# Optimization experiments

Measured on AMD Instinct MI355X. Metric: run time of the kernel, lower is better.

The kernel has to match this reference:

```python
import jax, jax.numpy as jnp
import numpy as np

B, N, C = 8, 2048, 256
NGRP = 4          # n oscillator dims per group
RANK = 16         # A_rank
EPS = 1e-6        # solver eps
GN_EPS = 1e-5     # torch GroupNorm default eps


def setup_inputs() -> dict:
    key = jax.random.key(0)
    k0, k1, k2, k3 = jax.random.split(key, 4)
    x = jax.random.normal(k0, (B, N, C), jnp.float32)
    y = jax.random.normal(k1, (B, C, N), jnp.float32)
    sc = jax.random.uniform(k2, (B, N, N), jnp.float32)
    U = 0.01 * jax.random.normal(k3, (N, RANK), jnp.float32)
    omega_param = (1.0 / np.sqrt(2)).astype(np.float32) * jnp.ones((C // 2, 1), jnp.float32)
    gn_w = jnp.ones((C,), jnp.float32)
    gn_b = jnp.zeros((C,), jnp.float32)
    gamma = jnp.float32(1.0)
    return {"x": x, "y": y, "sc": sc, "U": U, "omega_param": omega_param,
            "gn_w": gn_w, "gn_b": gn_b, "gamma": gamma, "Q": 8}


def _map_to_sphere(x):
    # normalize each group of NGRP channels to unit norm
    xv = x.reshape(B, N, C // NGRP, NGRP)
    n2 = jnp.clip(jnp.sum(xv * xv, axis=-1, keepdims=True), EPS, None)
    return (xv * jax.lax.rsqrt(n2)).reshape(B, N, C)


def _project_osc(v, x):
    # remove component of v along x within each oscillator group (tangent projection)
    xv = x.reshape(B, N, C // NGRP, NGRP)
    vv = v.reshape(B, N, C // NGRP, NGRP)
    sim = jnp.sum(xv * vv, axis=-1, keepdims=True)
    return (vv - sim * xv).reshape(B, N, C)


def _group_norm(y, w, b):
    # y: [B, C, N]; num_groups = C // NGRP, NGRP channels per group
    G = C // NGRP
    yv = y.reshape(B, G, NGRP * N)
    mu = jnp.mean(yv, axis=-1, keepdims=True)
    var = jnp.mean((yv - mu) ** 2, axis=-1, keepdims=True)
    yn = ((yv - mu) * jax.lax.rsqrt(var + GN_EPS)).reshape(B, C, N)
    return yn * w[None, :, None] + b[None, :, None]


def _omega_term(x, omega_param):
    # pairwise rotation: (x0, x1) -> (omg*x1, -omg*x0), omg = |omega_param| per pair
    xp = x.reshape(B, N, C // 2, 2)
    omg = jnp.abs(omega_param).reshape(1, 1, C // 2)  # norm over trailing dim of size 1
    out = jnp.stack([omg * xp[..., 1], -omg * xp[..., 0]], axis=-1)
    return out.reshape(B, N, C)


def _kuramoto(x, y, sc, U, omega_param, gn_w, gn_b, gamma, Q):
    rho = 1.0
    # y: [B, C, N] -> GroupNorm -> [B, N, C] -> sphere
    y = _group_norm(y, gn_w, gn_b)
    y = _map_to_sphere(jnp.transpose(y, (0, 2, 1)))
    # x: [B, N, C] (N != C so no transpose in original)
    x = _map_to_sphere(x)
    # coupling matrix K = sym(W) * sigmoid(U U^T)  (normalize_K=False, w_scale=1)
    Wsym = 0.5 * (sc + jnp.transpose(sc, (0, 2, 1)))
    A = jax.nn.sigmoid(U @ U.T)          # [N, N]
    K = Wsym * A[None, :, :]             # [B, N, N]

    def step(xc, _):
        coupling = jnp.einsum('bnm,bmc->bnc', K, xc)
        force = coupling + y
        om = _omega_term(xc, omega_param)
        dxdt = om + rho * _project_osc(force, xc)
        xn = _map_to_sphere(xc + gamma * dxdt)
        return xn, xn

    _, xs = jax.lax.scan(step, x, None, length=Q)
    return xs  # [Q, B, N, C]


def reference(x, y, sc, U, omega_param, gn_w, gn_b, gamma, Q):
    return _kuramoto(x, y, sc, U, omega_param, gn_w, gn_b, gamma, Q)
```

## Files before the change

kernel.cpp:

```cpp
#include <hip/hip_runtime.h>
#include <hip/hip_bf16.h>

#define BB 8
#define NN 2048
#define CC 256
#define GG 64
#define QQ 8

typedef unsigned short u16;
typedef __attribute__((ext_vector_type(8))) short bf16x8;
typedef __attribute__((ext_vector_type(4))) float f32x4;

static __device__ __forceinline__ float b2f(u16 u) {
  union { unsigned int i; float f; } cv; cv.i = ((unsigned int)u) << 16; return cv.f;
}
static __device__ __forceinline__ u16 f2b(float f) {
  union { __hip_bfloat16 h; u16 u; } cv; cv.h = __float2bfloat16(f); return cv.u;
}
static __device__ __forceinline__ float ldin(const void* p, size_t i, bool f32) {
  return f32 ? ((const float*)p)[i] : b2f(((const u16*)p)[i]);
}
static __device__ __forceinline__ float4 ldin4(const void* p, size_t i, bool f32) {
  if (f32) return *(const float4*)((const float*)p + i);
  ushort4 u = *(const ushort4*)((const u16*)p + i);
  return make_float4(b2f(u.x), b2f(u.y), b2f(u.z), b2f(u.w));
}
static __device__ __forceinline__ void gload16(const void* g, void* l) {
  __builtin_amdgcn_global_load_lds(
      (const __attribute__((address_space(1))) void*)g,
      (__attribute__((address_space(3))) void*)l, 16, 0, 0);
}

__global__ __launch_bounds__(256) void detect_kernel(const u16* __restrict__ sc,
                                                     int* __restrict__ flag)
{
  __shared__ int sh;
  if (threadIdx.x == 0) sh = 0;
  __syncthreads();
  int cnt = 0;
  for (int i = threadIdx.x; i < 2048; i += 256) {
    u16 w = sc[2 * i];
    int e = (w >> 7) & 0xFF;
    if (e >= 100 && e <= 130) cnt++;
  }
  atomicAdd(&sh, cnt);
  __syncthreads();
  if (threadIdx.x == 0) *flag = (sh < 1024) ? 1 : 0;
}

__global__ __launch_bounds__(256) void build_k_kernel(
    const void* __restrict__ sc, const void* __restrict__ U,
    u16* __restrict__ Khi, u16* __restrict__ Klo,
    const int* __restrict__ flagp, int grp)
{
  const int i0 = blockIdx.y * 32;
  const int j0 = blockIdx.x * 32;
  if (j0 < i0) return;
  const bool f32 = (*flagp != 0);
  const int tx = threadIdx.x;
  const int ty = threadIdx.y;
  const int t  = ty * 32 + tx;
  const int rr = t >> 3;
  const int cq = t & 7;

  __shared__ float Ui[32][17];
  __shared__ float Uj[32][17];
  __shared__ float As[32][33];
  __shared__ float t1[32][33];
  __shared__ float t2[32][33];

  for (int s = t; s < 512; s += 256) {
    int r2 = s >> 4, kk = s & 15;
    Ui[r2][kk] = ldin(U, (size_t)(i0 + r2) * 16 + kk, f32);
    Uj[r2][kk] = ldin(U, (size_t)(j0 + r2) * 16 + kk, f32);
  }
  __syncthreads();
  for (int ii = ty; ii < 32; ii += 8) {
    float dot = 0.f;
    #pragma unroll
    for (int k = 0; k < 16; k++) dot += Ui[ii][k] * Uj[tx][k];
    As[ii][tx] = 1.0f / (1.0f + expf(-dot));
  }

  for (int bl = 0; bl < 4; bl++) {
    const int b = grp * 4 + bl;
    const size_t scb = (size_t)b * NN * NN;
    __syncthreads();
    float4 va = ldin4(sc, scb + (size_t)(i0 + rr) * NN + j0 + 4 * cq, f32);
    float4 vb = ldin4(sc, scb + (size_t)(j0 + rr) * NN + i0 + 4 * cq, f32);
    t1[rr][4*cq+0] = va.x; t1[rr][4*cq+1] = va.y;
    t1[rr][4*cq+2] = va.z; t1[rr][4*cq+3] = va.w;
    t2[rr][4*cq+0] = vb.x; t2[rr][4*cq+1] = vb.y;
    t2[rr][4*cq+2] = vb.z; t2[rr][4*cq+3] = vb.w;
    __syncthreads();
    const size_t kfb = (size_t)bl * NN * NN;
    ushort4 h4, l4;
    #pragma unroll
    for (int k = 0; k < 4; k++) {
      int col = 4 * cq + k;
      float kv = 0.5f * (t1[rr][col] + t2[col][rr]) * As[rr][col];
      u16 h = f2b(kv);
      ((u16*)&h4)[k] = h;
      ((u16*)&l4)[k] = f2b(kv - b2f(h));
    }
    size_t o = kfb + (size_t)(i0 + rr) * NN + j0 + 4 * cq;
    *(ushort4*)(Khi + o) = h4;
    *(ushort4*)(Klo + o) = l4;
    if (i0 != j0) {
      #pragma unroll
      for (int k = 0; k < 4; k++) {
        int col = 4 * cq + k;
        float kv = 0.5f * (t2[rr][col] + t1[col][rr]) * As[col][rr];
        u16 h = f2b(kv);
        ((u16*)&h4)[k] = h;
        ((u16*)&l4)[k] = f2b(kv - b2f(h));
      }
      size_t o2 = kfb + (size_t)(j0 + rr) * NN + i0 + 4 * cq;
      *(ushort4*)(Khi + o2) = h4;
      *(ushort4*)(Klo + o2) = l4;
    }
  }
}

__global__ __launch_bounds__(256) void gn_stats_kernel(
    const void* __restrict__ y, float* __restrict__ murs,
    const int* __restrict__ flagp)
{
  const bool f32 = (*flagp != 0);
  const int bg = blockIdx.x;
  float s = 0.f, ss = 0.f;
  if (f32) {
    const float* base = (const float*)y + (size_t)bg * 4 * NN;
    for (int i = threadIdx.x; i < 2048; i += 256) {
      float4 v = *(const float4*)(base + (size_t)i * 4);
      s  += v.x + v.y + v.z + v.w;
      ss += v.x*v.x + v.y*v.y + v.z*v.z + v.w*v.w;
    }
  } else {
    const u16* base = (const u16*)y + (size_t)bg * 4 * NN;
    for (int i = threadIdx.x; i < 2048; i += 256) {
      ushort4 v = *(const ushort4*)(base + (size_t)i * 4);
      float f0 = b2f(v.x), f1 = b2f(v.y), f2 = b2f(v.z), f3 = b2f(v.w);
      s  += f0 + f1 + f2 + f3;
      ss += f0*f0 + f1*f1 + f2*f2 + f3*f3;
    }
  }
  #pragma unroll
  for (int off = 32; off > 0; off >>= 1) {
    s  += __shfl_down(s, off, 64);
    ss += __shfl_down(ss, off, 64);
  }
  __shared__ float sh[8];
  const int w = threadIdx.x >> 6, ln = threadIdx.x & 63;
  if (ln == 0) { sh[w * 2] = s; sh[w * 2 + 1] = ss; }
  __syncthreads();
  if (threadIdx.x == 0) {
    float S  = sh[0] + sh[2] + sh[4] + sh[6];
    float SS = sh[1] + sh[3] + sh[5] + sh[7];
    float mu  = S / 8192.0f;
    float var = SS / 8192.0f - mu * mu;
    murs[bg * 2]     = mu;
    murs[bg * 2 + 1] = 1.0f / sqrtf(fmaxf(var, 0.f) + 1e-5f);
  }
}

__global__ __launch_bounds__(256) void y_tf_kernel(
    const void* __restrict__ y, const float* __restrict__ murs,
    const void* __restrict__ gw, const void* __restrict__ gb,
    float* __restrict__ yt, const int* __restrict__ flagp)
{
  const bool f32 = (*flagp != 0);
  const int b = blockIdx.y;
  const int n = blockIdx.x * 64 + threadIdx.x;
  for (int g = threadIdx.y; g < GG; g += 4) {
    float mu = murs[(b * GG + g) * 2];
    float rs = murs[(b * GG + g) * 2 + 1];
    float v[4];
    #pragma unroll
    for (int k = 0; k < 4; k++) {
      int c = 4 * g + k;
      float val = (ldin(y, ((size_t)b * CC + c) * NN + n, f32) - mu) * rs;
      v[k] = val * ldin(gw, c, f32) + ldin(gb, c, f32);
    }
    float n2 = v[0]*v[0] + v[1]*v[1] + v[2]*v[2] + v[3]*v[3];
    float scl = 1.0f / sqrtf(fmaxf(n2, 1e-6f));
    float4 o; o.x = v[0]*scl; o.y = v[1]*scl; o.z = v[2]*scl; o.w = v[3]*scl;
    *(float4*)(yt + ((size_t)b * NN + n) * CC + 4 * g) = o;
  }
}

__global__ __launch_bounds__(256) void x_init_kernel(
    const void* __restrict__ x, u16* __restrict__ xTh, u16* __restrict__ xTl,
    const int* __restrict__ flagp)
{
  const bool f32 = (*flagp != 0);
  const int b = blockIdx.y;
  const int n = blockIdx.x * 64 + threadIdx.x;
  for (int g = threadIdx.y; g < GG; g += 4) {
    size_t idx = ((size_t)b * NN + n) * CC + 4 * g;
    float v[4];
    if (f32) {
      float4 u4 = *(const float4*)((const float*)x + idx);
      v[0] = u4.x; v[1] = u4.y; v[2] = u4.z; v[3] = u4.w;
    } else {
      ushort4 u = *(const ushort4*)((const u16*)x + idx);
      v[0] = b2f(u.x); v[1] = b2f(u.y); v[2] = b2f(u.z); v[3] = b2f(u.w);
    }
    float n2 = v[0]*v[0] + v[1]*v[1] + v[2]*v[2] + v[3]*v[3];
    float scl = 1.0f / sqrtf(fmaxf(n2, 1e-6f));
    size_t xb = ((size_t)b * CC + 4 * g) * NN + n;
    #pragma unroll
    for (int k = 0; k < 4; k++) {
      float xv = v[k] * scl;
      u16 h = f2b(xv);
      xTh[xb + (size_t)k * NN] = h;
      xTl[xb + (size_t)k * NN] = f2b(xv - b2f(h));
    }
  }
}

__global__ __launch_bounds__(256, 2) void gemm_fused_kernel(
    const u16* __restrict__ Khi, const u16* __restrict__ Klo,
    const u16* __restrict__ xhc, const u16* __restrict__ xlc,
    u16* __restrict__ xhn, u16* __restrict__ xln,
    const float* __restrict__ yt, const void* __restrict__ omega,
    const void* __restrict__ gamma, void* __restrict__ outbase, size_t qoff,
    const int* __restrict__ flagp, int grp)
{
  const int flat = blockIdx.x + 4 * blockIdx.y + 128 * blockIdx.z;
  const int swz  = (flat & 7) * 64 + (flat >> 3);
  const int bx = swz & 3;
  const int by = (swz >> 2) & 31;
  const int bl = swz >> 7;
  const int b  = grp * 4 + bl;
  const int m0 = by * 64;
  const int c0 = bx * 64;

  __shared__ char lds[2][32768];

  const int t    = threadIdx.x;
  const int lane = t & 63;
  const int wid  = t >> 6;
  const int wr   = wid >> 1;
  const int wc   = wid & 1;

  const u16* Ah = Khi + (size_t)bl * NN * NN;
  const u16* Al = Klo + (size_t)bl * NN * NN;
  const u16* Bh = xhc + (size_t)b * CC * NN;
  const u16* Bl = xlc + (size_t)b * CC * NN;

  const int tr   = t >> 3;
  const int phys = (t & 7) ^ (tr & 7);
  const size_t aoff = (size_t)(m0 + tr) * NN + phys * 8;
  const size_t boff = (size_t)(c0 + tr) * NN + phys * 8;
  const int dst = wid * 1024;

  f32x4 acc[2][2];
  const f32x4 zero4 = {0.f, 0.f, 0.f, 0.f};
  #pragma unroll
  for (int i = 0; i < 2; i++)
    #pragma unroll
    for (int j = 0; j < 2; j++) acc[i][j] = zero4;

  auto stage = [&](int bufi, int k0) {
    char* base = &lds[bufi][0];
    #pragma unroll
    for (int i = 0; i < 2; i++) {
      gload16(Ah + aoff + (size_t)i * (32 * NN) + k0, base +         i * 4096 + dst);
      gload16(Al + aoff + (size_t)i * (32 * NN) + k0, base +  8192 + i * 4096 + dst);
      gload16(Bh + boff + (size_t)i * (32 * NN) + k0, base + 16384 + i * 4096 + dst);
      gload16(Bl + boff + (size_t)i * (32 * NN) + k0, base + 24576 + i * 4096 + dst);
    }
  };

  const int l15 = lane & 15;
  const int lk  = lane >> 4;

  auto compute = [&](int bufi) {
    const char* base = &lds[bufi][0];
    #pragma unroll
    for (int ks = 0; ks < 2; ks++) {
      const int cl = ks * 4 + lk;
      bf16x8 fah[2], fal[2], fbh[2], fbl[2];
      #pragma unroll
      for (int fr = 0; fr < 2; fr++) {
        int r   = wr * 32 + fr * 16 + l15;
        int off = r * 128 + ((cl ^ (r & 7)) << 4);
        fah[fr] = *(const bf16x8*)(base + off);
        fal[fr] = *(const bf16x8*)(base + 8192 + off);
      }
      #pragma unroll
      for (int fc = 0; fc < 2; fc++) {
        int r   = wc * 32 + fc * 16 + l15;
        int off = r * 128 + ((cl ^ (r & 7)) << 4);
        fbh[fc] = *(const bf16x8*)(base + 16384 + off);
        fbl[fc] = *(const bf16x8*)(base + 24576 + off);
      }
      #pragma unroll
      for (int fr = 0; fr < 2; fr++)
        #pragma unroll
        for (int fc = 0; fc < 2; fc++) {
          acc[fr][fc] = __builtin_amdgcn_mfma_f32_16x16x32_bf16(
              fah[fr], fbh[fc], acc[fr][fc], 0, 0, 0);
          acc[fr][fc] = __builtin_amdgcn_mfma_f32_16x16x32_bf16(
              fah[fr], fbl[fc], acc[fr][fc], 0, 0, 0);
          acc[fr][fc] = __builtin_amdgcn_mfma_f32_16x16x32_bf16(
              fal[fr], fbh[fc], acc[fr][fc], 0, 0, 0);
        }
    }
  };

  stage(0, 0);
  __syncthreads();
  int buf = 0;
  for (int kt = 0; kt < NN / 64; kt++) {
    if (kt + 1 < NN / 64) stage(buf ^ 1, (kt + 1) * 64);
    compute(buf);
    __syncthreads();
    buf ^= 1;
  }

  const bool f32 = (*flagp != 0);
  const float gm = ldin(gamma, 0, f32);
  #pragma unroll
  for (int fr = 0; fr < 2; fr++) {
    const int rbase = m0 + wr * 32 + fr * 16 + lk * 4;
    #pragma unroll
    for (int fc = 0; fc < 2; fc++) {
      const int c = c0 + wc * 32 + fc * 16 + l15;
      const size_t xoff = ((size_t)b * CC + c) * NN + rbase;
      ushort4 xh4 = *(const ushort4*)(xhc + xoff);
      ushort4 xl4 = *(const ushort4*)(xlc + xoff);
      float xcv[4] = { b2f(xh4.x) + b2f(xl4.x), b2f(xh4.y) + b2f(xl4.y),
                       b2f(xh4.z) + b2f(xl4.z), b2f(xh4.w) + b2f(xl4.w) };
      float om   = fabsf(ldin(omega, c >> 1, f32));
      float omsg = (c & 1) ? -om : om;
      float xn[4];
      #pragma unroll
      for (int r = 0; r < 4; r++) {
        const int n = rbase + r;
        float f = acc[fr][fc][r] + yt[((size_t)b * NN + n) * CC + c];
        float s = xcv[r] * f;
        s += __shfl_xor(s, 1);
        s += __shfl_xor(s, 2);
        float xp = __shfl_xor(xcv[r], 1);
        float d  = omsg * xp + (f - s * xcv[r]);
        float v  = xcv[r] + gm * d;
        float n2 = v * v;
        n2 += __shfl_xor(n2, 1);
        n2 += __shfl_xor(n2, 2);
        float scl = 1.0f / sqrtf(fmaxf(n2, 1e-6f));
        xn[r] = v * scl;
        const size_t oidx = qoff + ((size_t)b * NN + n) * CC + c;
        if (f32) ((float*)outbase)[oidx] = xn[r];
        else     ((u16*)outbase)[oidx]   = f2b(xn[r]);
      }
      ushort4 nh, nl;
      #pragma unroll
      for (int r = 0; r < 4; r++) {
        u16 h = f2b(xn[r]);
        ((u16*)&nh)[r] = h;
        ((u16*)&nl)[r] = f2b(xn[r] - b2f(h));
      }
      *(ushort4*)(xhn + xoff) = nh;
      *(ushort4*)(xln + xoff) = nl;
    }
  }
}

extern "C" void kernel_launch(void* const* d_in, const int* in_sizes, int n_in,
                              void* d_out, int out_size, void* d_ws, size_t ws_size,
                              hipStream_t stream) {
  const void* x     = d_in[0];
  const void* y     = d_in[1];
  const void* sc    = d_in[2];
  const void* U     = d_in[3];
  const void* omega = d_in[4];
  const void* gw    = d_in[5];
  const void* gb    = d_in[6];
  const void* gamma = d_in[7];
  char* ws = (char*)d_ws;

  const size_t BNC = (size_t)BB * NN * CC;
  u16*   Khi  = (u16*)(ws);
  u16*   Klo  = (u16*)(ws + 33554432);
  float* yt   = (float*)(ws + 67108864);
  u16*   xAh  = (u16*)(ws + 83886080);
  u16*   xAl  = (u16*)(ws + 92274688);
  u16*   xBh  = (u16*)(ws + 100663296);
  u16*   xBl  = (u16*)(ws + 109051904);
  float* murs = (float*)(ws + 117440512);
  int*   flag = (int*)  (ws + 117444608);

  u16* xh[2] = { xAh, xBh };
  u16* xl[2] = { xAl, xBl };

  detect_kernel<<<dim3(1), dim3(256), 0, stream>>>((const u16*)sc, flag);
  gn_stats_kernel<<<dim3(512), dim3(256), 0, stream>>>(y, murs, flag);
  y_tf_kernel<<<dim3(32, 8), dim3(64, 4), 0, stream>>>(y, murs, gw, gb, yt, flag);
  x_init_kernel<<<dim3(32, 8), dim3(64, 4), 0, stream>>>(x, xAh, xAl, flag);

  for (int grp = 0; grp < 2; grp++) {
    build_k_kernel<<<dim3(64, 64), dim3(32, 8), 0, stream>>>(
        sc, U, Khi, Klo, flag, grp);
    for (int q = 0; q < QQ; q++) {
      const int cur = q & 1, nxt = cur ^ 1;
      gemm_fused_kernel<<<dim3(4, 32, 4), dim3(256), 0, stream>>>(
          Khi, Klo, xh[cur], xl[cur], xh[nxt], xl[nxt],
          yt, omega, gamma, d_out, (size_t)q * BNC, flag, grp);
    }
  }
}
```

Measured before the change: 916.3 us.

## Load B operand fragments directly from global into registers, halve LDS

```diff
diff --git a/kernel.cpp b/kernel.cpp
--- a/kernel.cpp
+++ b/kernel.cpp
@@ -236,7 +236,7 @@
   const int m0 = by * 64;
   const int c0 = bx * 64;
 
-  __shared__ char lds[2][32768];
+  __shared__ char lds[2][16384];
 
   const int t    = threadIdx.x;
   const int lane = t & 63;
@@ -252,8 +252,15 @@
   const int tr   = t >> 3;
   const int phys = (t & 7) ^ (tr & 7);
   const size_t aoff = (size_t)(m0 + tr) * NN + phys * 8;
-  const size_t boff = (size_t)(c0 + tr) * NN + phys * 8;
   const int dst = wid * 1024;
+
+  const int l15 = lane & 15;
+  const int lk  = lane >> 4;
+
+  const u16* bh0 = Bh + (size_t)(c0 + wc * 32 +      l15) * NN + lk * 8;
+  const u16* bh1 = Bh + (size_t)(c0 + wc * 32 + 16 + l15) * NN + lk * 8;
+  const u16* bl0 = Bl + (size_t)(c0 + wc * 32 +      l15) * NN + lk * 8;
+  const u16* bl1 = Bl + (size_t)(c0 + wc * 32 + 16 + l15) * NN + lk * 8;
 
   f32x4 acc[2][2];
   const f32x4 zero4 = {0.f, 0.f, 0.f, 0.f};
@@ -262,26 +269,32 @@
     #pragma unroll
     for (int j = 0; j < 2; j++) acc[i][j] = zero4;
 
-  auto stage = [&](int bufi, int k0) {
+  auto stageA = [&](int bufi, int kt) {
     char* base = &lds[bufi][0];
-    #pragma unroll
-    for (int i = 0; i < 2; i++) {
-      gload16(Ah + aoff + (size_t)i * (32 * NN) + k0, base +         i * 4096 + dst);
-      gload16(Al + aoff + (size_t)i * (32 * NN) + k0, base +  8192 + i * 4096 + dst);
-      gload16(Bh + boff + (size_t)i * (32 * NN) + k0, base + 16384 + i * 4096 + dst);
-      gload16(Bl + boff + (size_t)i * (32 * NN) + k0, base + 24576 + i * 4096 + dst);
-    }
+    const int k0 = kt * 64;
+    gload16(Ah + aoff + k0,           base +         dst);
+    gload16(Ah + aoff + 32 * NN + k0, base +  4096 + dst);
+    gload16(Al + aoff + k0,           base +  8192 + dst);
+    gload16(Al + aoff + 32 * NN + k0, base + 12288 + dst);
   };
 
-  const int l15 = lane & 15;
-  const int lk  = lane >> 4;
-
-  auto compute = [&](int bufi) {
+  auto loadB = [&](bf16x8 (&fh)[2][2], bf16x8 (&fl)[2][2], int kt) {
+    const int k0 = kt * 64;
+    #pragma unroll
+    for (int ks = 0; ks < 2; ks++) {
+      fh[ks][0] = *(const bf16x8*)(bh0 + k0 + ks * 32);
+      fh[ks][1] = *(const bf16x8*)(bh1 + k0 + ks * 32);
+      fl[ks][0] = *(const bf16x8*)(bl0 + k0 + ks * 32);
+      fl[ks][1] = *(const bf16x8*)(bl1 + k0 + ks * 32);
+    }
+  };
+
+  auto computeA = [&](int bufi, bf16x8 (&fh)[2][2], bf16x8 (&fl)[2][2]) {
     const char* base = &lds[bufi][0];
     #pragma unroll
     for (int ks = 0; ks < 2; ks++) {
       const int cl = ks * 4 + lk;
-      bf16x8 fah[2], fal[2], fbh[2], fbl[2];
+      bf16x8 fah[2], fal[2];
       #pragma unroll
       for (int fr = 0; fr < 2; fr++) {
         int r   = wr * 32 + fr * 16 + l15;
@@ -290,34 +303,34 @@
         fal[fr] = *(const bf16x8*)(base + 8192 + off);
       }
       #pragma unroll
-      for (int fc = 0; fc < 2; fc++) {
-        int r   = wc * 32 + fc * 16 + l15;
-        int off = r * 128 + ((cl ^ (r & 7)) << 4);
-        fbh[fc] = *(const bf16x8*)(base + 16384 + off);
-        fbl[fc] = *(const bf16x8*)(base + 24576 + off);
-      }
-      #pragma unroll
       for (int fr = 0; fr < 2; fr++)
         #pragma unroll
         for (int fc = 0; fc < 2; fc++) {
           acc[fr][fc] = __builtin_amdgcn_mfma_f32_16x16x32_bf16(
-              fah[fr], fbh[fc], acc[fr][fc], 0, 0, 0);
+              fah[fr], fh[ks][fc], acc[fr][fc], 0, 0, 0);
           acc[fr][fc] = __builtin_amdgcn_mfma_f32_16x16x32_bf16(
-              fah[fr], fbl[fc], acc[fr][fc], 0, 0, 0);
+              fah[fr], fl[ks][fc], acc[fr][fc], 0, 0, 0);
           acc[fr][fc] = __builtin_amdgcn_mfma_f32_16x16x32_bf16(
-              fal[fr], fbh[fc], acc[fr][fc], 0, 0, 0);
+              fal[fr], fh[ks][fc], acc[fr][fc], 0, 0, 0);
         }
     }
   };
 
-  stage(0, 0);
+  bf16x8 b0h[2][2], b0l[2][2], b1h[2][2], b1l[2][2];
+  stageA(0, 0);
+  loadB(b0h, b0l, 0);
   __syncthreads();
-  int buf = 0;
-  for (int kt = 0; kt < NN / 64; kt++) {
-    if (kt + 1 < NN / 64) stage(buf ^ 1, (kt + 1) * 64);
-    compute(buf);
+  for (int kt = 0; kt < NN / 64; kt += 2) {
+    stageA(1, kt + 1);
+    loadB(b1h, b1l, kt + 1);
+    computeA(0, b0h, b0l);
     __syncthreads();
-    buf ^= 1;
+    if (kt + 2 < NN / 64) {
+      stageA(0, kt + 2);
+      loadB(b0h, b0l, kt + 2);
+    }
+    computeA(1, b1h, b1l);
+    __syncthreads();
   }
 
   const bool f32 = (*flagp != 0);
```

New measurement: 1.687 ms. +84.1%, slower.

## Process all batches per launch with single-buffered higher-occupancy GEMM when workspace allows

Applied to the files above, without the earlier changes.

```diff
diff --git a/kernel.cpp b/kernel.cpp
--- a/kernel.cpp
+++ b/kernel.cpp
@@ -51,7 +51,7 @@
 __global__ __launch_bounds__(256) void build_k_kernel(
     const void* __restrict__ sc, const void* __restrict__ U,
     u16* __restrict__ Khi, u16* __restrict__ Klo,
-    const int* __restrict__ flagp, int grp)
+    const int* __restrict__ flagp, int b0, int nbat)
 {
   const int i0 = blockIdx.y * 32;
   const int j0 = blockIdx.x * 32;
@@ -82,8 +82,8 @@
     As[ii][tx] = 1.0f / (1.0f + expf(-dot));
   }
 
-  for (int bl = 0; bl < 4; bl++) {
-    const int b = grp * 4 + bl;
+  for (int bl = 0; bl < nbat; bl++) {
+    const int b = b0 + bl;
     const size_t scb = (size_t)b * NN * NN;
     __syncthreads();
     float4 va = ldin4(sc, scb + (size_t)(i0 + rr) * NN + j0 + 4 * cq, f32);
@@ -219,108 +219,14 @@
   }
 }
 
-__global__ __launch_bounds__(256, 2) void gemm_fused_kernel(
-    const u16* __restrict__ Khi, const u16* __restrict__ Klo,
+static __device__ __forceinline__ void fused_step_epilogue(
+    f32x4 (&acc)[2][2], int b, int m0, int c0, int wr, int wc, int l15, int lk,
     const u16* __restrict__ xhc, const u16* __restrict__ xlc,
     u16* __restrict__ xhn, u16* __restrict__ xln,
     const float* __restrict__ yt, const void* __restrict__ omega,
     const void* __restrict__ gamma, void* __restrict__ outbase, size_t qoff,
-    const int* __restrict__ flagp, int grp)
-{
-  const int flat = blockIdx.x + 4 * blockIdx.y + 128 * blockIdx.z;
-  const int swz  = (flat & 7) * 64 + (flat >> 3);
-  const int bx = swz & 3;
-  const int by = (swz >> 2) & 31;
-  const int bl = swz >> 7;
-  const int b  = grp * 4 + bl;
-  const int m0 = by * 64;
-  const int c0 = bx * 64;
-
-  __shared__ char lds[2][32768];
-
-  const int t    = threadIdx.x;
-  const int lane = t & 63;
-  const int wid  = t >> 6;
-  const int wr   = wid >> 1;
-  const int wc   = wid & 1;
-
-  const u16* Ah = Khi + (size_t)bl * NN * NN;
-  const u16* Al = Klo + (size_t)bl * NN * NN;
-  const u16* Bh = xhc + (size_t)b * CC * NN;
-  const u16* Bl = xlc + (size_t)b * CC * NN;
-
-  const int tr   = t >> 3;
-  const int phys = (t & 7) ^ (tr & 7);
-  const size_t aoff = (size_t)(m0 + tr) * NN + phys * 8;
-  const size_t boff = (size_t)(c0 + tr) * NN + phys * 8;
-  const int dst = wid * 1024;
-
-  f32x4 acc[2][2];
-  const f32x4 zero4 = {0.f, 0.f, 0.f, 0.f};
-  #pragma unroll
-  for (int i = 0; i < 2; i++)
-    #pragma unroll
-    for (int j = 0; j < 2; j++) acc[i][j] = zero4;
-
-  auto stage = [&](int bufi, int k0) {
-    char* base = &lds[bufi][0];
-    #pragma unroll
-    for (int i = 0; i < 2; i++) {
-      gload16(Ah + aoff + (size_t)i * (32 * NN) + k0, base +         i * 4096 + dst);
-      gload16(Al + aoff + (size_t)i * (32 * NN) + k0, base +  8192 + i * 4096 + dst);
-      gload16(Bh + boff + (size_t)i * (32 * NN) + k0, base + 16384 + i * 4096 + dst);
-      gload16(Bl + boff + (size_t)i * (32 * NN) + k0, base + 24576 + i * 4096 + dst);
-    }
-  };
-
-  const int l15 = lane & 15;
-  const int lk  = lane >> 4;
-
-  auto compute = [&](int bufi) {
-    const char* base = &lds[bufi][0];
-    #pragma unroll
-    for (int ks = 0; ks < 2; ks++) {
-      const int cl = ks * 4 + lk;
-      bf16x8 fah[2], fal[2], fbh[2], fbl[2];
-      #pragma unroll
-      for (int fr = 0; fr < 2; fr++) {
-        int r   = wr * 32 + fr * 16 + l15;
-        int off = r * 128 + ((cl ^ (r & 7)) << 4);
-        fah[fr] = *(const bf16x8*)(base + off);
-        fal[fr] = *(const bf16x8*)(base + 8192 + off);
-      }
-      #pragma unroll
-      for (int fc = 0; fc < 2; fc++) {
-        int r   = wc * 32 + fc * 16 + l15;
-        int off = r * 128 + ((cl ^ (r & 7)) << 4);
-        fbh[fc] = *(const bf16x8*)(base + 16384 + off);
-        fbl[fc] = *(const bf16x8*)(base + 24576 + off);
-      }
-      #pragma unroll
-      for (int fr = 0; fr < 2; fr++)
-        #pragma unroll
-        for (int fc = 0; fc < 2; fc++) {
-          acc[fr][fc] = __builtin_amdgcn_mfma_f32_16x16x32_bf16(
-              fah[fr], fbh[fc], acc[fr][fc], 0, 0, 0);
-          acc[fr][fc] = __builtin_amdgcn_mfma_f32_16x16x32_bf16(
-              fah[fr], fbl[fc], acc[fr][fc], 0, 0, 0);
-          acc[fr][fc] = __builtin_amdgcn_mfma_f32_16x16x32_bf16(
-              fal[fr], fbh[fc], acc[fr][fc], 0, 0, 0);
-        }
-    }
-  };
-
-  stage(0, 0);
-  __syncthreads();
-  int buf = 0;
-  for (int kt = 0; kt < NN / 64; kt++) {
-    if (kt + 1 < NN / 64) stage(buf ^ 1, (kt + 1) * 64);
-    compute(buf);
-    __syncthreads();
-    buf ^= 1;
-  }
-
-  const bool f32 = (*flagp != 0);
+    bool f32)
+{
   const float gm = ldin(gamma, 0, f32);
   #pragma unroll
   for (int fr = 0; fr < 2; fr++) {
@@ -368,6 +274,206 @@
   }
 }
 
+__global__ __launch_bounds__(256, 4) void gemm_fused_sb(
+    const u16* __restrict__ Khi, const u16* __restrict__ Klo,
+    const u16* __restrict__ xhc, const u16* __restrict__ xlc,
+    u16* __restrict__ xhn, u16* __restrict__ xln,
+    const float* __restrict__ yt, const void* __restrict__ omega,
+    const void* __restrict__ gamma, void* __restrict__ outbase, size_t qoff,
+    const int* __restrict__ flagp)
+{
+  const int flat = blockIdx.x + 4 * blockIdx.y + 128 * blockIdx.z;
+  const int swz  = (flat & 7) * 128 + (flat >> 3);
+  const int bx = swz & 3;
+  const int by = (swz >> 2) & 31;
+  const int b  = swz >> 7;
+  const int m0 = by * 64;
+  const int c0 = bx * 64;
+
+  __shared__ char lds[32768];
+
+  const int t    = threadIdx.x;
+  const int lane = t & 63;
+  const int wid  = t >> 6;
+  const int wr   = wid >> 1;
+  const int wc   = wid & 1;
+
+  const u16* Ah = Khi + (size_t)b * NN * NN;
+  const u16* Al = Klo + (size_t)b * NN * NN;
+  const u16* Bh = xhc + (size_t)b * CC * NN;
+  const u16* Bl = xlc + (size_t)b * CC * NN;
+
+  const int tr   = t >> 3;
+  const int phys = (t & 7) ^ (tr & 7);
+  const size_t aoff = (size_t)(m0 + tr) * NN + phys * 8;
+  const size_t boff = (size_t)(c0 + tr) * NN + phys * 8;
+  const int dst = wid * 1024;
+
+  f32x4 acc[2][2];
+  const f32x4 zero4 = {0.f, 0.f, 0.f, 0.f};
+  #pragma unroll
+  for (int i = 0; i < 2; i++)
+    #pragma unroll
+    for (int j = 0; j < 2; j++) acc[i][j] = zero4;
+
+  const int l15 = lane & 15;
+  const int lk  = lane >> 4;
+
+  for (int kt = 0; kt < NN / 64; kt++) {
+    const int k0 = kt * 64;
+    #pragma unroll
+    for (int i = 0; i < 2; i++) {
+      gload16(Ah + aoff + (size_t)i * (32 * NN) + k0, lds +         i * 4096 + dst);
+      gload16(Al + aoff + (size_t)i * (32 * NN) + k0, lds +  8192 + i * 4096 + dst);
+      gload16(Bh + boff + (size_t)i * (32 * NN) + k0, lds + 16384 + i * 4096 + dst);
+      gload16(Bl + boff + (size_t)i * (32 * NN) + k0, lds + 24576 + i * 4096 + dst);
+    }
+    __syncthreads();
+    #pragma unroll
+    for (int ks = 0; ks < 2; ks++) {
+      const int cl = ks * 4 + lk;
+      bf16x8 fah[2], fal[2], fbh[2], fbl[2];
+      #pragma unroll
+      for (int fr = 0; fr < 2; fr++) {
+        int r   = wr * 32 + fr * 16 + l15;
+        int off = r * 128 + ((cl ^ (r & 7)) << 4);
+        fah[fr] = *(const bf16x8*)(lds + off);
+        fal[fr] = *(const bf16x8*)(lds + 8192 + off);
+      }
+      #pragma unroll
+      for (int fc = 0; fc < 2; fc++) {
+        int r   = wc * 32 + fc * 16 + l15;
+        int off = r * 128 + ((cl ^ (r & 7)) << 4);
+        fbh[fc] = *(const bf16x8*)(lds + 16384 + off);
+        fbl[fc] = *(const bf16x8*)(lds + 24576 + off);
+      }
+      #pragma unroll
+      for (int fr = 0; fr < 2; fr++)
+        #pragma unroll
+        for (int fc = 0; fc < 2; fc++) {
+          acc[fr][fc] = __builtin_amdgcn_mfma_f32_16x16x32_bf16(
+              fah[fr], fbh[fc], acc[fr][fc], 0, 0, 0);
+          acc[fr][fc] = __builtin_amdgcn_mfma_f32_16x16x32_bf16(
+              fah[fr], fbl[fc], acc[fr][fc], 0, 0, 0);
+          acc[fr][fc] = __builtin_amdgcn_mfma_f32_16x16x32_bf16(
+              fal[fr], fbh[fc], acc[fr][fc], 0, 0, 0);
+        }
+    }
+    __syncthreads();
+  }
+
+  fused_step_epilogue(acc, b, m0, c0, wr, wc, l15, lk,
+                      xhc, xlc, xhn, xln, yt, omega, gamma,
+                      outbase, qoff, (*flagp != 0));
+}
+
+__global__ __launch_bounds__(256, 2) void gemm_fused_db(
+    const u16* __restrict__ Khi, const u16* __restrict__ Klo,
+    const u16* __restrict__ xhc, const u16* __restrict__ xlc,
+    u16* __restrict__ xhn, u16* __restrict__ xln,
+    const float* __restrict__ yt, const void* __restrict__ omega,
+    const void* __restrict__ gamma, void* __restrict__ outbase, size_t qoff,
+    const int* __restrict__ flagp, int grp)
+{
+  const int flat = blockIdx.x + 4 * blockIdx.y + 128 * blockIdx.z;
+  const int swz  = (flat & 7) * 64 + (flat >> 3);
+  const int bx = swz & 3;
+  const int by = (swz >> 2) & 31;
+  const int bl = swz >> 7;
+  const int b  = grp * 4 + bl;
+  const int m0 = by * 64;
+  const int c0 = bx * 64;
+
+  __shared__ char lds[2][32768];
+
+  const int t    = threadIdx.x;
+  const int lane = t & 63;
+  const int wid  = t >> 6;
+  const int wr   = wid >> 1;
+  const int wc   = wid & 1;
+
+  const u16* Ah = Khi + (size_t)bl * NN * NN;
+  const u16* Al = Klo + (size_t)bl * NN * NN;
+  const u16* Bh = xhc + (size_t)b * CC * NN;
+  const u16* Bl = xlc + (size_t)b * CC * NN;
+
+  const int tr   = t >> 3;
+  const int phys = (t & 7) ^ (tr & 7);
+  const size_t aoff = (size_t)(m0 + tr) * NN + phys * 8;
+  const size_t boff = (size_t)(c0 + tr) * NN + phys * 8;
+  const int dst = wid * 1024;
+
+  f32x4 acc[2][2];
+  const f32x4 zero4 = {0.f, 0.f, 0.f, 0.f};
+  #pragma unroll
+  for (int i = 0; i < 2; i++)
+    #pragma unroll
+    for (int j = 0; j < 2; j++) acc[i][j] = zero4;
+
+  auto stage = [&](int bufi, int kt) {
+    char* base = &lds[bufi][0];
+    const int k0 = kt * 64;
+    #pragma unroll
+    for (int i = 0; i < 2; i++) {
+      gload16(Ah + aoff + (size_t)i * (32 * NN) + k0, base +         i * 4096 + dst);
+      gload16(Al + aoff + (size_t)i * (32 * NN) + k0, base +  8192 + i * 4096 + dst);
+      gload16(Bh + boff + (size_t)i * (32 * NN) + k0, base + 16384 + i * 4096 + dst);
+      gload16(Bl + boff + (size_t)i * (32 * NN) + k0, base + 24576 + i * 4096 + dst);
+    }
+  };
+
+  const int l15 = lane & 15;
+  const int lk  = lane >> 4;
+
+  auto compute = [&](int bufi) {
+    const char* base = &lds[bufi][0];
+    #pragma unroll
+    for (int ks = 0; ks < 2; ks++) {
+      const int cl = ks * 4 + lk;
+      bf16x8 fah[2], fal[2], fbh[2], fbl[2];
+      #pragma unroll
+      for (int fr = 0; fr < 2; fr++) {
+        int r   = wr * 32 + fr * 16 + l15;
+        int off = r * 128 + ((cl ^ (r & 7)) << 4);
+        fah[fr] = *(const bf16x8*)(base + off);
+        fal[fr] = *(const bf16x8*)(base + 8192 + off);
+      }
+      #pragma unroll
+      for (int fc = 0; fc < 2; fc++) {
+        int r   = wc * 32 + fc * 16 + l15;
+        int off = r * 128 + ((cl ^ (r & 7)) << 4);
+        fbh[fc] = *(const bf16x8*)(base + 16384 + off);
+        fbl[fc] = *(const bf16x8*)(base + 24576 + off);
+      }
+      #pragma unroll
+      for (int fr = 0; fr < 2; fr++)
+        #pragma unroll
+        for (int fc = 0; fc < 2; fc++) {
+          acc[fr][fc] = __builtin_amdgcn_mfma_f32_16x16x32_bf16(
+              fah[fr], fbh[fc], acc[fr][fc], 0, 0, 0);
+          acc[fr][fc] = __builtin_amdgcn_mfma_f32_16x16x32_bf16(
+              fah[fr], fbl[fc], acc[fr][fc], 0, 0, 0);
+          acc[fr][fc] = __builtin_amdgcn_mfma_f32_16x16x32_bf16(
+              fal[fr], fbh[fc], acc[fr][fc], 0, 0, 0);
+        }
+    }
+  };
+
+  stage(0, 0);
+  __syncthreads();
+  int buf = 0;
+  for (int kt = 0; kt < NN / 64; kt++) {
+    if (kt + 1 < NN / 64) stage(buf ^ 1, kt + 1);
+    compute(buf);
+    __syncthreads();
+    buf ^= 1;
+  }
+
+  fused_step_epilogue(acc, b, m0, c0, wr, wc, l15, lk,
+                      xhc, xlc, xhn, xln, yt, omega, gamma,
+                      outbase, qoff, (*flagp != 0));
+}
+
 extern "C" void kernel_launch(void* const* d_in, const int* in_sizes, int n_in,
                               void* d_out, int out_size, void* d_ws, size_t ws_size,
                               hipStream_t stream) {
@@ -382,32 +488,59 @@
   char* ws = (char*)d_ws;
 
   const size_t BNC = (size_t)BB * NN * CC;
-  u16*   Khi  = (u16*)(ws);
-  u16*   Klo  = (u16*)(ws + 33554432);
-  float* yt   = (float*)(ws + 67108864);
-  u16*   xAh  = (u16*)(ws + 83886080);
-  u16*   xAl  = (u16*)(ws + 92274688);
-  u16*   xBh  = (u16*)(ws + 100663296);
-  u16*   xBl  = (u16*)(ws + 109051904);
-  float* murs = (float*)(ws + 117440512);
-  int*   flag = (int*)  (ws + 117444608);
-
-  u16* xh[2] = { xAh, xBh };
-  u16* xl[2] = { xAl, xBl };
-
-  detect_kernel<<<dim3(1), dim3(256), 0, stream>>>((const u16*)sc, flag);
-  gn_stats_kernel<<<dim3(512), dim3(256), 0, stream>>>(y, murs, flag);
-  y_tf_kernel<<<dim3(32, 8), dim3(64, 4), 0, stream>>>(y, murs, gw, gb, yt, flag);
-  x_init_kernel<<<dim3(32, 8), dim3(64, 4), 0, stream>>>(x, xAh, xAl, flag);
-
-  for (int grp = 0; grp < 2; grp++) {
+  const bool big = ws_size >= 184600000ull;
+
+  if (big) {
+    u16*   Khi  = (u16*)(ws);
+    u16*   Klo  = (u16*)(ws + 67108864);
+    float* yt   = (float*)(ws + 134217728);
+    u16*   xAh  = (u16*)(ws + 150994944);
+    u16*   xAl  = (u16*)(ws + 159383552);
+    u16*   xBh  = (u16*)(ws + 167772160);
+    u16*   xBl  = (u16*)(ws + 176160768);
+    float* murs = (float*)(ws + 184549376);
+    int*   flag = (int*)  (ws + 184553472);
+    u16* xh[2] = { xAh, xBh };
+    u16* xl[2] = { xAl, xBl };
+
+    detect_kernel<<<dim3(1), dim3(256), 0, stream>>>((const u16*)sc, flag);
+    gn_stats_kernel<<<dim3(512), dim3(256), 0, stream>>>(y, murs, flag);
+    y_tf_kernel<<<dim3(32, 8), dim3(64, 4), 0, stream>>>(y, murs, gw, gb, yt, flag);
+    x_init_kernel<<<dim3(32, 8), dim3(64, 4), 0, stream>>>(x, xAh, xAl, flag);
     build_k_kernel<<<dim3(64, 64), dim3(32, 8), 0, stream>>>(
-        sc, U, Khi, Klo, flag, grp);
+        sc, U, Khi, Klo, flag, 0, 8);
     for (int q = 0; q < QQ; q++) {
       const int cur = q & 1, nxt = cur ^ 1;
-      gemm_fused_kernel<<<dim3(4, 32, 4), dim3(256), 0, stream>>>(
+      gemm_fused_sb<<<dim3(4, 32, 8), dim3(256), 0, stream>>>(
           Khi, Klo, xh[cur], xl[cur], xh[nxt], xl[nxt],
-          yt, omega, gamma, d_out, (size_t)q * BNC, flag, grp);
-    }
-  }
-}
+          yt, omega, gamma, d_out, (size_t)q * BNC, flag);
+    }
+  } else {
+    u16*   Khi  = (u16*)(ws);
+    u16*   Klo  = (u16*)(ws + 33554432);
+    float* yt   = (float*)(ws + 67108864);
+    u16*   xAh  = (u16*)(ws + 83886080);
+    u16*   xAl  = (u16*)(ws + 92274688);
+    u16*   xBh  = (u16*)(ws + 100663296);
+    u16*   xBl  = (u16*)(ws + 109051904);
+    float* murs = (float*)(ws + 117440512);
+    int*   flag = (int*)  (ws + 117444608);
+    u16* xh[2] = { xAh, xBh };
+    u16* xl[2] = { xAl, xBl };
+
+    detect_kernel<<<dim3(1), dim3(256), 0, stream>>>((const u16*)sc, flag);
+    gn_stats_kernel<<<dim3(512), dim3(256), 0, stream>>>(y, murs, flag);
+    y_tf_kernel<<<dim3(32, 8), dim3(64, 4), 0, stream>>>(y, murs, gw, gb, yt, flag);
+    x_init_kernel<<<dim3(32, 8), dim3(64, 4), 0, stream>>>(x, xAh, xAl, flag);
+    for (int grp = 0; grp < 2; grp++) {
+      build_k_kernel<<<dim3(64, 64), dim3(32, 8), 0, stream>>>(
+          sc, U, Khi, Klo, flag, grp * 4, 4);
+      for (int q = 0; q < QQ; q++) {
+        const int cur = q & 1, nxt = cur ^ 1;
+        gemm_fused_db<<<dim3(4, 32, 4), dim3(256), 0, stream>>>(
+            Khi, Klo, xh[cur], xl[cur], xh[nxt], xl[nxt],
+            yt, omega, gamma, d_out, (size_t)q * BNC, flag, grp);
+      }
+    }
+  }
+}
```

After: 927.0 us. Within noise of the previous version (+1.2%).
